# Optimization experiments

Hardware: AMD Instinct MI355X
Metric: run time of the kernel (lower is better)

The kernel has to match this reference:

```python
import jax, jax.numpy as jnp
import numpy as np

N_NODES = 100000
N_EDGES = 3200000
N_GRAPHS = 1000
HID = 64
L = 4  # num_unit


def setup_inputs() -> dict:
    key = jax.random.key(0)
    ks = jax.random.split(key, 16)
    x = jax.random.normal(ks[0], (N_NODES, 4), dtype=jnp.float32)
    edge_index = jax.random.randint(ks[1], (2, N_EDGES), 0, N_NODES, dtype=jnp.int64)
    edge_attr = jax.random.uniform(ks[2], (N_EDGES,), dtype=jnp.float32)
    batch = jnp.sort(jax.random.randint(ks[3], (N_NODES,), 0, N_GRAPHS, dtype=jnp.int64))
    s = 1.0 / np.sqrt(HID)
    inp = {
        'x': x, 'edge_index': edge_index, 'edge_attr': edge_attr, 'batch': batch,
        'emb_w': jax.random.normal(ks[4], (4, HID), jnp.float32) * 0.5,
        'emb_b': jnp.zeros((HID,), jnp.float32),
        'conv_w1': jax.random.normal(ks[5], (L, HID, HID), jnp.float32) * s,
        'conv_b1': jnp.zeros((L, HID), jnp.float32),
        'conv_w2': jax.random.normal(ks[6], (L, HID, HID), jnp.float32) * s,
        'conv_w3': jax.random.normal(ks[7], (L, HID, HID), jnp.float32) * s,
        'conv_b3': jnp.zeros((L, HID), jnp.float32),
        'lin1_w': jax.random.normal(ks[8], (HID, HID), jnp.float32) * s,
        'lin1_b': jnp.zeros((HID,), jnp.float32),
        'lin2_w': jax.random.normal(ks[9], (HID, 3), jnp.float32) * s,
        'lin2_b': jnp.zeros((3,), jnp.float32),
    }
    return inp


def _forward(x, edge_index, edge_attr, batch,
             emb_w, emb_b, conv_w1, conv_b1, conv_w2, conv_w3, conv_b3,
             lin1_w, lin1_b, lin2_w, lin2_b):
    src, dst = edge_index[0], edge_index[1]
    ew = edge_attr[:, None]  # [E,1]
    h = x @ emb_w + emb_b  # node_emb; dropout omitted (eval mode)
    for l in range(conv_w1.shape[0]):
        # LEConv: out_i = sum_{j->i} w_ji * (lin1(x_j) - lin2(x_i)) + lin3(x_i)
        a = h @ conv_w1[l] + conv_b1[l]
        b = h @ conv_w2[l]  # no bias
        msg = (a[src] - b[dst]) * ew  # [E, HID]
        agg = jax.ops.segment_sum(msg, dst, num_segments=h.shape[0])
        h = jax.nn.relu(agg + h @ conv_w3[l] + conv_b3[l])
    # global mean pool over graphs
    sums = jax.ops.segment_sum(h, batch, num_segments=N_GRAPHS)
    cnt = jax.ops.segment_sum(jnp.ones((h.shape[0],), h.dtype), batch, num_segments=N_GRAPHS)
    graph_x = sums / jnp.maximum(cnt, 1.0)[:, None]
    pred = jax.nn.relu(graph_x @ lin1_w + lin1_b) @ lin2_w + lin2_b
    return pred


def reference(x, edge_index, edge_attr, batch, emb_w, emb_b,
              conv_w1, conv_b1, conv_w2, conv_w3, conv_b3,
              lin1_w, lin1_b, lin2_w, lin2_b):
    return _forward(x, edge_index, edge_attr, batch, emb_w, emb_b,
                    conv_w1, conv_b1, conv_w2, conv_w3, conv_b3,
                    lin1_w, lin1_b, lin2_w, lin2_b)
```

## Files before the change

kernel.cpp:

```cpp
#include <hip/hip_runtime.h>

#define N_NODES 100000
#define N_EDGES 3200000
#define N_GRAPHS 1000
#define NLAYER 4
#define NB 391
#define G1 782
#define EPB 4096
#define PCAP 16384

typedef __attribute__((ext_vector_type(8))) short bf16x8;
typedef __attribute__((ext_vector_type(4))) float f32x4;

static __device__ __forceinline__ unsigned f2bf(float f) {
  unsigned u = __float_as_uint(f);
  return (u + 0x7fffu + ((u >> 16) & 1u)) >> 16;
}

__global__ __launch_bounds__(256) void embed_kernel(
    const float* __restrict__ x, const float* __restrict__ emb_w,
    const float* __restrict__ emb_b, float* __restrict__ h,
    unsigned short* __restrict__ h_bf)
{
  int t = blockIdx.x * 256 + threadIdx.x;
  if (t >= N_NODES * 64) return;
  int c = t & 63, v = t >> 6;
  float4 xv = ((const float4*)x)[v];
  float acc = emb_b[c];
  acc = fmaf(xv.x, emb_w[0 * 64 + c], acc);
  acc = fmaf(xv.y, emb_w[1 * 64 + c], acc);
  acc = fmaf(xv.z, emb_w[2 * 64 + c], acc);
  acc = fmaf(xv.w, emb_w[3 * 64 + c], acc);
  h[t] = acc;
  h_bf[t] = (unsigned short)f2bf(acc);
}

__global__ __launch_bounds__(256) void bhist_kernel(
    const int* __restrict__ ei, int* __restrict__ bhist)
{
  __shared__ unsigned hist[NB];
  for (int i = threadIdx.x; i < NB; i += 256) hist[i] = 0;
  __syncthreads();
  int base = blockIdx.x * EPB;
#pragma unroll
  for (int i = 0; i < 16; ++i) {
    int e = base + i * 256 + threadIdx.x;
    if (e < N_EDGES) atomicAdd(&hist[((unsigned)ei[N_EDGES + e]) >> 8], 1u);
  }
  __syncthreads();
  for (int i = threadIdx.x; i < NB; i += 256)
    bhist[blockIdx.x * NB + i] = (int)hist[i];
}

__global__ __launch_bounds__(256) void colscan_kernel(
    int* __restrict__ bhist, int* __restrict__ tots)
{
  int b = blockIdx.x;
  __shared__ int s[256];
  __shared__ int carry;
  if (threadIdx.x == 0) carry = 0;
  __syncthreads();
  for (int c0 = 0; c0 < G1; c0 += 256) {
    int g = c0 + threadIdx.x;
    int v = (g < G1) ? bhist[g * NB + b] : 0;
    s[threadIdx.x] = v;
    __syncthreads();
    for (int off = 1; off < 256; off <<= 1) {
      int y = (threadIdx.x >= off) ? s[threadIdx.x - off] : 0;
      __syncthreads();
      s[threadIdx.x] += y;
      __syncthreads();
    }
    if (g < G1) bhist[g * NB + b] = carry + s[threadIdx.x] - v;
    __syncthreads();
    if (threadIdx.x == 0) carry += s[255];
    __syncthreads();
  }
  if (threadIdx.x == 0) tots[b] = carry;
}

__global__ __launch_bounds__(512) void bucketscan_kernel(
    const int* __restrict__ tots, int* __restrict__ bb)
{
  __shared__ int s[512];
  int x = ((int)threadIdx.x < NB) ? tots[threadIdx.x] : 0;
  s[threadIdx.x] = x;
  __syncthreads();
  for (int off = 1; off < 512; off <<= 1) {
    int y = (threadIdx.x >= off) ? s[threadIdx.x - off] : 0;
    __syncthreads();
    s[threadIdx.x] += y;
    __syncthreads();
  }
  if ((int)threadIdx.x < NB) bb[threadIdx.x] = s[threadIdx.x] - x;
  if (threadIdx.x == 0) bb[NB] = N_EDGES;
}

__global__ __launch_bounds__(256) void bscatter_kernel(
    const int* __restrict__ ei, const float* __restrict__ ea,
    const int* __restrict__ bhist, const int* __restrict__ bb,
    int2* __restrict__ tmp)
{
  __shared__ unsigned hist[NB];
  __shared__ int lbase[NB];
  __shared__ unsigned cur[NB];
  __shared__ int2 stage[EPB];
  __shared__ unsigned short bid[EPB];
  __shared__ int carry;
  __shared__ int sbuf[256];
  int tid = threadIdx.x;
  int base = blockIdx.x * EPB;

  for (int i = tid; i < NB; i += 256) hist[i] = 0;
  if (tid == 0) carry = 0;
  __syncthreads();

#pragma unroll
  for (int i = 0; i < 16; ++i) {
    int e = base + i * 256 + tid;
    if (e < N_EDGES) atomicAdd(&hist[((unsigned)ei[N_EDGES + e]) >> 8], 1u);
  }
  __syncthreads();

  for (int c0 = 0; c0 < NB; c0 += 256) {
    int g = c0 + tid;
    int v = (g < NB) ? (int)hist[g] : 0;
    sbuf[tid] = v;
    __syncthreads();
    for (int off = 1; off < 256; off <<= 1) {
      int y = (tid >= off) ? sbuf[tid - off] : 0;
      __syncthreads();
      sbuf[tid] += y;
      __syncthreads();
    }
    if (g < NB) {
      int ex = carry + sbuf[tid] - v;
      lbase[g] = ex;
      cur[g] = (unsigned)ex;
    }
    __syncthreads();
    if (tid == 0) carry += sbuf[255];
    __syncthreads();
  }

#pragma unroll
  for (int i = 0; i < 16; ++i) {
    int e = base + i * 256 + tid;
    if (e < N_EDGES) {
      int d = ei[N_EDGES + e];
      unsigned bkt = ((unsigned)d) >> 8;
      unsigned lp = atomicAdd(&cur[bkt], 1u);
      stage[lp] = make_int2(ei[e] | ((d & 255) << 17), __float_as_int(ea[e]));
      bid[lp] = (unsigned short)bkt;
    }
  }
  __syncthreads();

  int nE = min(EPB, N_EDGES - base);
  for (int i = tid; i < nE; i += 256) {
    int bkt = (int)bid[i];
    int gpos = bb[bkt] + bhist[blockIdx.x * NB + bkt] + (i - lbase[bkt]);
    tmp[gpos] = stage[i];
  }
}

__global__ __launch_bounds__(256) void bucket_sort_kernel(
    const int* __restrict__ bb, const int2* __restrict__ tmp,
    int2* __restrict__ csr, int* __restrict__ row_off, float* __restrict__ degw)
{
  int j = blockIdx.x;
  int b0 = bb[j], b1 = bb[j + 1];
  int nE = b1 - b0;
  __shared__ unsigned hist[256];
  __shared__ float dws[256];
  __shared__ int scanbuf[256];
  __shared__ unsigned cur[256];
  __shared__ unsigned short perm[PCAP];
  int t = threadIdx.x;
  hist[t] = 0;
  dws[t] = 0.f;
  __syncthreads();
  for (int i = t; i < nE; i += 256) {
    int2 r = tmp[b0 + i];
    int bin = ((unsigned)r.x) >> 17;
    atomicAdd(&hist[bin], 1u);
    atomicAdd(&dws[bin], __int_as_float(r.y));
  }
  __syncthreads();
  int v = (int)hist[t];
  scanbuf[t] = v;
  __syncthreads();
  for (int off = 1; off < 256; off <<= 1) {
    int y = (t >= off) ? scanbuf[t - off] : 0;
    __syncthreads();
    scanbuf[t] += y;
    __syncthreads();
  }
  int myexcl = scanbuf[t] - v;
  cur[t] = (unsigned)myexcl;
  int vnode = (j << 8) + t;
  if (vnode < N_NODES) {
    row_off[vnode] = b0 + myexcl;
    degw[vnode] = dws[t];
  }
  if (j == NB - 1 && t == 0) row_off[N_NODES] = N_EDGES;
  __syncthreads();

  if (nE <= PCAP) {
    for (int i = t; i < nE; i += 256) {
      int2 r = tmp[b0 + i];
      int bin = ((unsigned)r.x) >> 17;
      unsigned p = atomicAdd(&cur[bin], 1u);
      perm[p] = (unsigned short)i;
    }
    __syncthreads();
    for (int q = t; q < nE; q += 256) {
      int2 r = tmp[b0 + (int)perm[q]];
      csr[b0 + q] = make_int2(r.x & 0x1FFFF, r.y);
    }
  } else {
    for (int i = t; i < nE; i += 256) {
      int2 r = tmp[b0 + i];
      int bin = ((unsigned)r.x) >> 17;
      unsigned p = atomicAdd(&cur[bin], 1u);
      csr[b0 + (int)p] = make_int2(r.x & 0x1FFFF, r.y);
    }
  }
}

__global__ __launch_bounds__(256) void matvec3_mfma_kernel(
    const unsigned short* __restrict__ h_bf,
    const float* __restrict__ w1, const float* __restrict__ b1,
    const float* __restrict__ w2,
    const float* __restrict__ w3, const float* __restrict__ b3,
    const float* __restrict__ degw,
    unsigned short* __restrict__ a_bf, float* __restrict__ cc_out)
{
  __shared__ unsigned wfrag[6144];
  int tid = threadIdx.x;
  {
    const float* wm0 = w2;
    const float* wm1 = w3;
    const float* wm2 = w1;
    for (int u = tid; u < 6144; u += 256) {
      int j2 = u & 3;
      int lane = (u >> 2) & 63;
      int t = (u >> 8) & 3;
      int c = (u >> 10) & 1;
      int m = u >> 11;
      int k = c * 32 + (lane >> 4) * 8 + j2 * 2;
      int n = t * 16 + (lane & 15);
      const float* W = (m == 0) ? wm0 : (m == 1) ? wm1 : wm2;
      unsigned lo = f2bf(W[k * 64 + n]);
      unsigned hi = f2bf(W[(k + 1) * 64 + n]);
      wfrag[u] = lo | (hi << 16);
    }
  }
  __syncthreads();

  int wave = tid >> 6;
  int lane = tid & 63;
  int quad = lane >> 4;
  int col = lane & 15;
  int nb = blockIdx.x * 64 + wave * 16;

  int arow = nb + col;
  if (arow >= N_NODES) arow = N_NODES - 1;
  const bf16x8* ap = (const bf16x8*)(h_bf + (size_t)arow * 64 + quad * 8);
  bf16x8 af0 = ap[0];
  bf16x8 af1 = ap[4];

  float dwr[4];
#pragma unroll
  for (int r = 0; r < 4; ++r) {
    int row = nb + quad * 4 + r;
    dwr[r] = degw[row < N_NODES ? row : 0];
  }

#pragma unroll
  for (int t = 0; t < 4; ++t) {
    const bf16x8* b20 = (const bf16x8*)&wfrag[((0 * 4 + t) << 8) + lane * 4];
    const bf16x8* b21 = (const bf16x8*)&wfrag[((1 * 4 + t) << 8) + lane * 4];
    const bf16x8* b30 = (const bf16x8*)&wfrag[((2 * 4 + t) << 8) + lane * 4];
    const bf16x8* b31 = (const bf16x8*)&wfrag[((3 * 4 + t) << 8) + lane * 4];
    const bf16x8* b10 = (const bf16x8*)&wfrag[((4 * 4 + t) << 8) + lane * 4];
    const bf16x8* b11 = (const bf16x8*)&wfrag[((5 * 4 + t) << 8) + lane * 4];

    f32x4 z = {0.f, 0.f, 0.f, 0.f};
    f32x4 acc2 = __builtin_amdgcn_mfma_f32_16x16x32_bf16(af0, *b20, z, 0, 0, 0);
    acc2 = __builtin_amdgcn_mfma_f32_16x16x32_bf16(af1, *b21, acc2, 0, 0, 0);
    f32x4 cc;
#pragma unroll
    for (int r = 0; r < 4; ++r) cc[r] = -dwr[r] * acc2[r];
    cc = __builtin_amdgcn_mfma_f32_16x16x32_bf16(af0, *b30, cc, 0, 0, 0);
    cc = __builtin_amdgcn_mfma_f32_16x16x32_bf16(af1, *b31, cc, 0, 0, 0);
    float bb3 = b3[t * 16 + col];
#pragma unroll
    for (int r = 0; r < 4; ++r) {
      int row = nb + quad * 4 + r;
      if (row < N_NODES) cc_out[(size_t)row * 64 + t * 16 + col] = cc[r] + bb3;
    }

    float bb1 = b1[t * 16 + col];
    f32x4 a1 = {bb1, bb1, bb1, bb1};
    a1 = __builtin_amdgcn_mfma_f32_16x16x32_bf16(af0, *b10, a1, 0, 0, 0);
    a1 = __builtin_amdgcn_mfma_f32_16x16x32_bf16(af1, *b11, a1, 0, 0, 0);
#pragma unroll
    for (int r = 0; r < 4; ++r) {
      int row = nb + quad * 4 + r;
      if (row < N_NODES)
        a_bf[(size_t)row * 64 + t * 16 + col] = (unsigned short)f2bf(a1[r]);
    }
  }
}

__global__ __launch_bounds__(256) void agg_kernel(
    const uint2* __restrict__ a2, const float4* __restrict__ cc4,
    const int* __restrict__ row_off, const int2* __restrict__ csr,
    float4* __restrict__ h4, unsigned short* __restrict__ h_bf)
{
  int wave = (blockIdx.x * 256 + threadIdx.x) >> 6;
  int lane = threadIdx.x & 63;
  int sg = lane >> 4;
  int li = lane & 15;
  int v = wave * 4 + sg;
  bool valid = v < N_NODES;
  int vc = valid ? v : N_NODES - 1;
  int base = row_off[vc];
  int ecnt = valid ? (row_off[vc + 1] - base) : 0;
  int emax = ecnt;
  emax = max(emax, __shfl_xor(emax, 16));
  emax = max(emax, __shfl_xor(emax, 32));

  float4 acc = valid ? cc4[(size_t)vc * 16 + li] : make_float4(0.f, 0.f, 0.f, 0.f);

  int full = emax & ~15;
  int c0 = 0;
  for (; c0 < full; c0 += 16) {
    int idx = c0 + li;
    int2 er = (idx < ecnt) ? csr[base + idx] : make_int2(0, 0);
#pragma unroll
    for (int j = 0; j < 16; ++j) {
      int sl = sg * 16 + j;
      int s = __shfl(er.x, sl);
      float w = __int_as_float(__shfl(er.y, sl));
      uint2 u = a2[(size_t)s * 16 + li];
      acc.x = fmaf(w, __uint_as_float(u.x << 16), acc.x);
      acc.y = fmaf(w, __uint_as_float(u.x & 0xffff0000u), acc.y);
      acc.z = fmaf(w, __uint_as_float(u.y << 16), acc.z);
      acc.w = fmaf(w, __uint_as_float(u.y & 0xffff0000u), acc.w);
    }
  }
  int rem = emax - full;
  if (rem > 0) {
    int idx = c0 + li;
    int2 er = (idx < ecnt) ? csr[base + idx] : make_int2(0, 0);
    for (int j = 0; j < rem; ++j) {
      int sl = sg * 16 + j;
      int s = __shfl(er.x, sl);
      float w = __int_as_float(__shfl(er.y, sl));
      uint2 u = a2[(size_t)s * 16 + li];
      acc.x = fmaf(w, __uint_as_float(u.x << 16), acc.x);
      acc.y = fmaf(w, __uint_as_float(u.x & 0xffff0000u), acc.y);
      acc.z = fmaf(w, __uint_as_float(u.y << 16), acc.z);
      acc.w = fmaf(w, __uint_as_float(u.y & 0xffff0000u), acc.w);
    }
  }
  if (valid) {
    acc.x = fmaxf(acc.x, 0.f);
    acc.y = fmaxf(acc.y, 0.f);
    acc.z = fmaxf(acc.z, 0.f);
    acc.w = fmaxf(acc.w, 0.f);
    h4[(size_t)v * 16 + li] = acc;
    uint2 p;
    p.x = f2bf(acc.x) | (f2bf(acc.y) << 16);
    p.y = f2bf(acc.z) | (f2bf(acc.w) << 16);
    ((uint2*)h_bf)[(size_t)v * 16 + li] = p;
  }
}

__global__ __launch_bounds__(256) void head_kernel(
    const float* __restrict__ h, const int* __restrict__ batch,
    const float* __restrict__ l1w, const float* __restrict__ l1b,
    const float* __restrict__ l2w, const float* __restrict__ l2b,
    float* __restrict__ out)
{
  int g = (blockIdx.x * 256 + threadIdx.x) >> 6;
  int lane = threadIdx.x & 63;
  if (g >= N_GRAPHS) return;
  int lo = 0, hi = N_NODES;
  while (lo < hi) { int mid = (lo + hi) >> 1; if (batch[mid] < g) lo = mid + 1; else hi = mid; }
  int start = lo;
  hi = N_NODES;
  while (lo < hi) { int mid = (lo + hi) >> 1; if (batch[mid] < g + 1) lo = mid + 1; else hi = mid; }
  int end = lo;

  float sum = 0.f;
  for (int v = start; v < end; ++v) sum += h[(size_t)v * 64 + lane];
  float cntf = (float)(end - start);
  float gx = sum / fmaxf(cntf, 1.f);

  float acc = l1b[lane];
  for (int k = 0; k < 64; ++k) {
    float gxk = __shfl(gx, k);
    acc = fmaf(gxk, l1w[k * 64 + lane], acc);
  }
  float t = fmaxf(acc, 0.f);
  float p0 = t * l2w[lane * 3 + 0];
  float p1 = t * l2w[lane * 3 + 1];
  float p2 = t * l2w[lane * 3 + 2];
  for (int off = 32; off > 0; off >>= 1) {
    p0 += __shfl_down(p0, off);
    p1 += __shfl_down(p1, off);
    p2 += __shfl_down(p2, off);
  }
  if (lane == 0) {
    out[g * 3 + 0] = p0 + l2b[0];
    out[g * 3 + 1] = p1 + l2b[1];
    out[g * 3 + 2] = p2 + l2b[2];
  }
}

extern "C" void kernel_launch(void* const* d_in, const int* in_sizes, int n_in,
                              void* d_out, int out_size, void* d_ws, size_t ws_size,
                              hipStream_t stream)
{
  (void)in_sizes; (void)n_in; (void)out_size; (void)ws_size;
  const float* x     = (const float*)d_in[0];
  const int*   ei    = (const int*)d_in[1];
  const float* ea    = (const float*)d_in[2];
  const int*   batch = (const int*)d_in[3];
  const float* emb_w = (const float*)d_in[4];
  const float* emb_b = (const float*)d_in[5];
  const float* cw1   = (const float*)d_in[6];
  const float* cb1   = (const float*)d_in[7];
  const float* cw2   = (const float*)d_in[8];
  const float* cw3   = (const float*)d_in[9];
  const float* cb3   = (const float*)d_in[10];
  const float* l1w   = (const float*)d_in[11];
  const float* l1b   = (const float*)d_in[12];
  const float* l2w   = (const float*)d_in[13];
  const float* l2b   = (const float*)d_in[14];
  float* out = (float*)d_out;

  char* wsb = (char*)d_ws;
  size_t off = 0;
  auto alloc = [&](size_t bytes) {
    char* p = wsb + off;
    off = (off + bytes + 255) & ~(size_t)255;
    return p;
  };
  float* h       = (float*)alloc(sizeof(float) * (size_t)N_NODES * 64);
  unsigned short* h_bf = (unsigned short*)alloc(sizeof(short) * (size_t)N_NODES * 64);
  unsigned short* a_bf = (unsigned short*)alloc(sizeof(short) * (size_t)N_NODES * 64);
  float* cc_buf  = (float*)alloc(sizeof(float) * (size_t)N_NODES * 64);
  int2*  csr     = (int2*)alloc(sizeof(int2) * (size_t)N_EDGES);
  int*   row_off = (int*)alloc(sizeof(int) * (N_NODES + 1));
  float* degw    = (float*)alloc(sizeof(float) * N_NODES);
  int*   bhist   = (int*)alloc(sizeof(int) * (size_t)G1 * NB);
  int*   tots    = (int*)alloc(sizeof(int) * NB);
  int*   bb      = (int*)alloc(sizeof(int) * (NB + 1));
  int2* tmp = (int2*)cc_buf;

  embed_kernel<<<(N_NODES * 64 + 255) / 256, 256, 0, stream>>>(x, emb_w, emb_b, h, h_bf);
  bhist_kernel<<<G1, 256, 0, stream>>>(ei, bhist);
  colscan_kernel<<<NB, 256, 0, stream>>>(bhist, tots);
  bucketscan_kernel<<<1, 512, 0, stream>>>(tots, bb);
  bscatter_kernel<<<G1, 256, 0, stream>>>(ei, ea, bhist, bb, tmp);
  bucket_sort_kernel<<<NB, 256, 0, stream>>>(bb, tmp, csr, row_off, degw);

  int agg_blocks = (N_NODES + 15) / 16;
  int mv_blocks = (N_NODES + 63) / 64;
  for (int l = 0; l < NLAYER; ++l) {
    matvec3_mfma_kernel<<<mv_blocks, 256, 0, stream>>>(
        h_bf, cw1 + l * 4096, cb1 + l * 64, cw2 + l * 4096, cw3 + l * 4096,
        cb3 + l * 64, degw, a_bf, cc_buf);
    agg_kernel<<<agg_blocks, 256, 0, stream>>>(
        (const uint2*)a_bf, (const float4*)cc_buf, row_off, csr, (float4*)h, h_bf);
  }

  head_kernel<<<(N_GRAPHS * 64 + 255) / 256, 256, 0, stream>>>(
      h, batch, l1w, l1b, l2w, l2b, out);
}
```

Before: 625.4 us.

## Pack CSR edges into 32-bit words, store cc in bf16, trim fp32 h writes

Each CSR edge is packed into one 32-bit word: a 17-bit source index plus the edge weight quantized to 15 bits. This halves the edge-stream bytes read per layer. The cc buffer is stored as bf16 instead of fp32, and the fp32 h is written only in the last layer. The matvec kernel now covers 256 rows per block to amortize the weight-fragment setup, and that setup loop is restructured for coalesced weight reads. The 15-bit weight quantization and bf16 cc add precision loss relative to the fp32 reference, which may affect tolerance.

```diff
diff --git a/kernel.cpp b/kernel.cpp
--- a/kernel.cpp
+++ b/kernel.cpp
@@ -16,11 +16,16 @@
   unsigned u = __float_as_uint(f);
   return (u + 0x7fffu + ((u >> 16) & 1u)) >> 16;
 }
+static __device__ __forceinline__ float bf2f_lo(unsigned u) {
+  return __uint_as_float(u << 16);
+}
+static __device__ __forceinline__ float bf2f_hi(unsigned u) {
+  return __uint_as_float(u & 0xffff0000u);
+}
 
 __global__ __launch_bounds__(256) void embed_kernel(
     const float* __restrict__ x, const float* __restrict__ emb_w,
-    const float* __restrict__ emb_b, float* __restrict__ h,
-    unsigned short* __restrict__ h_bf)
+    const float* __restrict__ emb_b, unsigned short* __restrict__ h_bf)
 {
   int t = blockIdx.x * 256 + threadIdx.x;
   if (t >= N_NODES * 64) return;
@@ -31,7 +36,6 @@
   acc = fmaf(xv.y, emb_w[1 * 64 + c], acc);
   acc = fmaf(xv.z, emb_w[2 * 64 + c], acc);
   acc = fmaf(xv.w, emb_w[3 * 64 + c], acc);
-  h[t] = acc;
   h_bf[t] = (unsigned short)f2bf(acc);
 }
 
@@ -166,7 +170,7 @@
 
 __global__ __launch_bounds__(256) void bucket_sort_kernel(
     const int* __restrict__ bb, const int2* __restrict__ tmp,
-    int2* __restrict__ csr, int* __restrict__ row_off, float* __restrict__ degw)
+    unsigned* __restrict__ csr, int* __restrict__ row_off, float* __restrict__ degw)
 {
   int j = blockIdx.x;
   int b0 = bb[j], b1 = bb[j + 1];
@@ -216,14 +220,16 @@
     __syncthreads();
     for (int q = t; q < nE; q += 256) {
       int2 r = tmp[b0 + (int)perm[q]];
-      csr[b0 + q] = make_int2(r.x & 0x1FFFF, r.y);
+      unsigned q15 = (unsigned)(__int_as_float(r.y) * 32768.0f);
+      csr[b0 + q] = ((unsigned)r.x & 0x1FFFFu) | (q15 << 17);
     }
   } else {
     for (int i = t; i < nE; i += 256) {
       int2 r = tmp[b0 + i];
       int bin = ((unsigned)r.x) >> 17;
       unsigned p = atomicAdd(&cur[bin], 1u);
-      csr[b0 + (int)p] = make_int2(r.x & 0x1FFFF, r.y);
+      unsigned q15 = (unsigned)(__int_as_float(r.y) * 32768.0f);
+      csr[b0 + (int)p] = ((unsigned)r.x & 0x1FFFFu) | (q15 << 17);
     }
   }
 }
@@ -234,26 +240,27 @@
     const float* __restrict__ w2,
     const float* __restrict__ w3, const float* __restrict__ b3,
     const float* __restrict__ degw,
-    unsigned short* __restrict__ a_bf, float* __restrict__ cc_out)
+    unsigned short* __restrict__ a_bf, unsigned short* __restrict__ cc_bf)
 {
   __shared__ unsigned wfrag[6144];
   int tid = threadIdx.x;
   {
-    const float* wm0 = w2;
-    const float* wm1 = w3;
-    const float* wm2 = w1;
-    for (int u = tid; u < 6144; u += 256) {
-      int j2 = u & 3;
-      int lane = (u >> 2) & 63;
-      int t = (u >> 8) & 3;
-      int c = (u >> 10) & 1;
-      int m = u >> 11;
-      int k = c * 32 + (lane >> 4) * 8 + j2 * 2;
-      int n = t * 16 + (lane & 15);
-      const float* W = (m == 0) ? wm0 : (m == 1) ? wm1 : wm2;
+    int n = tid & 63;
+    int gofs = tid >> 6;
+    for (int it = 0; it < 24; ++it) {
+      int g = it * 4 + gofs;
+      int m = g >> 5;
+      int kp = g & 31;
+      int k = kp * 2;
+      const float* W = (m == 0) ? w2 : (m == 1) ? w3 : w1;
       unsigned lo = f2bf(W[k * 64 + n]);
       unsigned hi = f2bf(W[(k + 1) * 64 + n]);
-      wfrag[u] = lo | (hi << 16);
+      int c = k >> 5;
+      int kk = k & 31;
+      int lane = ((kk >> 3) << 4) | (n & 15);
+      int j2 = (kk & 7) >> 1;
+      int t = n >> 4;
+      wfrag[(((m * 2 + c) * 4 + t) << 8) | (lane << 2) | j2] = lo | (hi << 16);
     }
   }
   __syncthreads();
@@ -262,62 +269,66 @@
   int lane = tid & 63;
   int quad = lane >> 4;
   int col = lane & 15;
-  int nb = blockIdx.x * 64 + wave * 16;
-
-  int arow = nb + col;
-  if (arow >= N_NODES) arow = N_NODES - 1;
-  const bf16x8* ap = (const bf16x8*)(h_bf + (size_t)arow * 64 + quad * 8);
-  bf16x8 af0 = ap[0];
-  bf16x8 af1 = ap[4];
-
-  float dwr[4];
-#pragma unroll
-  for (int r = 0; r < 4; ++r) {
-    int row = nb + quad * 4 + r;
-    dwr[r] = degw[row < N_NODES ? row : 0];
-  }
-
-#pragma unroll
-  for (int t = 0; t < 4; ++t) {
-    const bf16x8* b20 = (const bf16x8*)&wfrag[((0 * 4 + t) << 8) + lane * 4];
-    const bf16x8* b21 = (const bf16x8*)&wfrag[((1 * 4 + t) << 8) + lane * 4];
-    const bf16x8* b30 = (const bf16x8*)&wfrag[((2 * 4 + t) << 8) + lane * 4];
-    const bf16x8* b31 = (const bf16x8*)&wfrag[((3 * 4 + t) << 8) + lane * 4];
-    const bf16x8* b10 = (const bf16x8*)&wfrag[((4 * 4 + t) << 8) + lane * 4];
-    const bf16x8* b11 = (const bf16x8*)&wfrag[((5 * 4 + t) << 8) + lane * 4];
-
-    f32x4 z = {0.f, 0.f, 0.f, 0.f};
-    f32x4 acc2 = __builtin_amdgcn_mfma_f32_16x16x32_bf16(af0, *b20, z, 0, 0, 0);
-    acc2 = __builtin_amdgcn_mfma_f32_16x16x32_bf16(af1, *b21, acc2, 0, 0, 0);
-    f32x4 cc;
-#pragma unroll
-    for (int r = 0; r < 4; ++r) cc[r] = -dwr[r] * acc2[r];
-    cc = __builtin_amdgcn_mfma_f32_16x16x32_bf16(af0, *b30, cc, 0, 0, 0);
-    cc = __builtin_amdgcn_mfma_f32_16x16x32_bf16(af1, *b31, cc, 0, 0, 0);
-    float bb3 = b3[t * 16 + col];
+
+#pragma unroll
+  for (int tt = 0; tt < 4; ++tt) {
+    int nb = blockIdx.x * 256 + wave * 64 + tt * 16;
+    int arow = nb + col;
+    if (arow >= N_NODES) arow = N_NODES - 1;
+    const bf16x8* ap = (const bf16x8*)(h_bf + (size_t)arow * 64 + quad * 8);
+    bf16x8 af0 = ap[0];
+    bf16x8 af1 = ap[4];
+
+    float dwr[4];
 #pragma unroll
     for (int r = 0; r < 4; ++r) {
       int row = nb + quad * 4 + r;
-      if (row < N_NODES) cc_out[(size_t)row * 64 + t * 16 + col] = cc[r] + bb3;
-    }
-
-    float bb1 = b1[t * 16 + col];
-    f32x4 a1 = {bb1, bb1, bb1, bb1};
-    a1 = __builtin_amdgcn_mfma_f32_16x16x32_bf16(af0, *b10, a1, 0, 0, 0);
-    a1 = __builtin_amdgcn_mfma_f32_16x16x32_bf16(af1, *b11, a1, 0, 0, 0);
-#pragma unroll
-    for (int r = 0; r < 4; ++r) {
-      int row = nb + quad * 4 + r;
-      if (row < N_NODES)
-        a_bf[(size_t)row * 64 + t * 16 + col] = (unsigned short)f2bf(a1[r]);
+      dwr[r] = degw[row < N_NODES ? row : 0];
+    }
+
+#pragma unroll
+    for (int t = 0; t < 4; ++t) {
+      const bf16x8* b20 = (const bf16x8*)&wfrag[((0 * 4 + t) << 8) + lane * 4];
+      const bf16x8* b21 = (const bf16x8*)&wfrag[((1 * 4 + t) << 8) + lane * 4];
+      const bf16x8* b30 = (const bf16x8*)&wfrag[((2 * 4 + t) << 8) + lane * 4];
+      const bf16x8* b31 = (const bf16x8*)&wfrag[((3 * 4 + t) << 8) + lane * 4];
+      const bf16x8* b10 = (const bf16x8*)&wfrag[((4 * 4 + t) << 8) + lane * 4];
+      const bf16x8* b11 = (const bf16x8*)&wfrag[((5 * 4 + t) << 8) + lane * 4];
+
+      f32x4 z = {0.f, 0.f, 0.f, 0.f};
+      f32x4 acc2 = __builtin_amdgcn_mfma_f32_16x16x32_bf16(af0, *b20, z, 0, 0, 0);
+      acc2 = __builtin_amdgcn_mfma_f32_16x16x32_bf16(af1, *b21, acc2, 0, 0, 0);
+      f32x4 cc;
+#pragma unroll
+      for (int r = 0; r < 4; ++r) cc[r] = -dwr[r] * acc2[r];
+      cc = __builtin_amdgcn_mfma_f32_16x16x32_bf16(af0, *b30, cc, 0, 0, 0);
+      cc = __builtin_amdgcn_mfma_f32_16x16x32_bf16(af1, *b31, cc, 0, 0, 0);
+      float bb3 = b3[t * 16 + col];
+#pragma unroll
+      for (int r = 0; r < 4; ++r) {
+        int row = nb + quad * 4 + r;
+        if (row < N_NODES)
+          cc_bf[(size_t)row * 64 + t * 16 + col] = (unsigned short)f2bf(cc[r] + bb3);
+      }
+
+      float bb1 = b1[t * 16 + col];
+      f32x4 a1 = {bb1, bb1, bb1, bb1};
+      a1 = __builtin_amdgcn_mfma_f32_16x16x32_bf16(af0, *b10, a1, 0, 0, 0);
+      a1 = __builtin_amdgcn_mfma_f32_16x16x32_bf16(af1, *b11, a1, 0, 0, 0);
+#pragma unroll
+      for (int r = 0; r < 4; ++r) {
+        int row = nb + quad * 4 + r;
+        if (row < N_NODES)
+          a_bf[(size_t)row * 64 + t * 16 + col] = (unsigned short)f2bf(a1[r]);
+      }
     }
   }
 }
 
 __global__ __launch_bounds__(256) void agg_kernel(
-    const uint2* __restrict__ a2, const float4* __restrict__ cc4,
-    const int* __restrict__ row_off, const int2* __restrict__ csr,
-    float4* __restrict__ h4, unsigned short* __restrict__ h_bf)
+    const uint2* __restrict__ a2, const uint2* __restrict__ cc2,
+    const int* __restrict__ row_off, const unsigned* __restrict__ csr,
+    float4* __restrict__ h4, unsigned short* __restrict__ h_bf, int write_h)
 {
   int wave = (blockIdx.x * 256 + threadIdx.x) >> 6;
   int lane = threadIdx.x & 63;
@@ -332,38 +343,45 @@
   emax = max(emax, __shfl_xor(emax, 16));
   emax = max(emax, __shfl_xor(emax, 32));
 
-  float4 acc = valid ? cc4[(size_t)vc * 16 + li] : make_float4(0.f, 0.f, 0.f, 0.f);
+  float4 acc = make_float4(0.f, 0.f, 0.f, 0.f);
+  if (valid) {
+    uint2 cu = cc2[(size_t)vc * 16 + li];
+    acc.x = bf2f_lo(cu.x);
+    acc.y = bf2f_hi(cu.x);
+    acc.z = bf2f_lo(cu.y);
+    acc.w = bf2f_hi(cu.y);
+  }
 
   int full = emax & ~15;
   int c0 = 0;
   for (; c0 < full; c0 += 16) {
     int idx = c0 + li;
-    int2 er = (idx < ecnt) ? csr[base + idx] : make_int2(0, 0);
+    unsigned er = (idx < ecnt) ? csr[base + idx] : 0u;
 #pragma unroll
     for (int j = 0; j < 16; ++j) {
-      int sl = sg * 16 + j;
-      int s = __shfl(er.x, sl);
-      float w = __int_as_float(__shfl(er.y, sl));
+      unsigned r = (unsigned)__shfl((int)er, sg * 16 + j);
+      int s = (int)(r & 0x1FFFFu);
+      float w = (float)(r >> 17) * (1.0f / 32768.0f);
       uint2 u = a2[(size_t)s * 16 + li];
-      acc.x = fmaf(w, __uint_as_float(u.x << 16), acc.x);
-      acc.y = fmaf(w, __uint_as_float(u.x & 0xffff0000u), acc.y);
-      acc.z = fmaf(w, __uint_as_float(u.y << 16), acc.z);
-      acc.w = fmaf(w, __uint_as_float(u.y & 0xffff0000u), acc.w);
+      acc.x = fmaf(w, bf2f_lo(u.x), acc.x);
+      acc.y = fmaf(w, bf2f_hi(u.x), acc.y);
+      acc.z = fmaf(w, bf2f_lo(u.y), acc.z);
+      acc.w = fmaf(w, bf2f_hi(u.y), acc.w);
     }
   }
   int rem = emax - full;
   if (rem > 0) {
     int idx = c0 + li;
-    int2 er = (idx < ecnt) ? csr[base + idx] : make_int2(0, 0);
+    unsigned er = (idx < ecnt) ? csr[base + idx] : 0u;
     for (int j = 0; j < rem; ++j) {
-      int sl = sg * 16 + j;
-      int s = __shfl(er.x, sl);
-      float w = __int_as_float(__shfl(er.y, sl));
+      unsigned r = (unsigned)__shfl((int)er, sg * 16 + j);
+      int s = (int)(r & 0x1FFFFu);
+      float w = (float)(r >> 17) * (1.0f / 32768.0f);
       uint2 u = a2[(size_t)s * 16 + li];
-      acc.x = fmaf(w, __uint_as_float(u.x << 16), acc.x);
-      acc.y = fmaf(w, __uint_as_float(u.x & 0xffff0000u), acc.y);
-      acc.z = fmaf(w, __uint_as_float(u.y << 16), acc.z);
-      acc.w = fmaf(w, __uint_as_float(u.y & 0xffff0000u), acc.w);
+      acc.x = fmaf(w, bf2f_lo(u.x), acc.x);
+      acc.y = fmaf(w, bf2f_hi(u.x), acc.y);
+      acc.z = fmaf(w, bf2f_lo(u.y), acc.z);
+      acc.w = fmaf(w, bf2f_hi(u.y), acc.w);
     }
   }
   if (valid) {
@@ -371,7 +389,7 @@
     acc.y = fmaxf(acc.y, 0.f);
     acc.z = fmaxf(acc.z, 0.f);
     acc.w = fmaxf(acc.w, 0.f);
-    h4[(size_t)v * 16 + li] = acc;
+    if (write_h) h4[(size_t)v * 16 + li] = acc;
     uint2 p;
     p.x = f2bf(acc.x) | (f2bf(acc.y) << 16);
     p.y = f2bf(acc.z) | (f2bf(acc.w) << 16);
@@ -453,16 +471,16 @@
   float* h       = (float*)alloc(sizeof(float) * (size_t)N_NODES * 64);
   unsigned short* h_bf = (unsigned short*)alloc(sizeof(short) * (size_t)N_NODES * 64);
   unsigned short* a_bf = (unsigned short*)alloc(sizeof(short) * (size_t)N_NODES * 64);
-  float* cc_buf  = (float*)alloc(sizeof(float) * (size_t)N_NODES * 64);
-  int2*  csr     = (int2*)alloc(sizeof(int2) * (size_t)N_EDGES);
+  unsigned short* cc_bf = (unsigned short*)alloc(sizeof(short) * (size_t)N_NODES * 64);
+  unsigned* csr  = (unsigned*)alloc(sizeof(unsigned) * (size_t)N_EDGES);
   int*   row_off = (int*)alloc(sizeof(int) * (N_NODES + 1));
   float* degw    = (float*)alloc(sizeof(float) * N_NODES);
   int*   bhist   = (int*)alloc(sizeof(int) * (size_t)G1 * NB);
   int*   tots    = (int*)alloc(sizeof(int) * NB);
   int*   bb      = (int*)alloc(sizeof(int) * (NB + 1));
-  int2* tmp = (int2*)cc_buf;
-
-  embed_kernel<<<(N_NODES * 64 + 255) / 256, 256, 0, stream>>>(x, emb_w, emb_b, h, h_bf);
+  int2* tmp = (int2*)h;
+
+  embed_kernel<<<(N_NODES * 64 + 255) / 256, 256, 0, stream>>>(x, emb_w, emb_b, h_bf);
   bhist_kernel<<<G1, 256, 0, stream>>>(ei, bhist);
   colscan_kernel<<<NB, 256, 0, stream>>>(bhist, tots);
   bucketscan_kernel<<<1, 512, 0, stream>>>(tots, bb);
@@ -470,13 +488,14 @@
   bucket_sort_kernel<<<NB, 256, 0, stream>>>(bb, tmp, csr, row_off, degw);
 
   int agg_blocks = (N_NODES + 15) / 16;
-  int mv_blocks = (N_NODES + 63) / 64;
+  int mv_blocks = (N_NODES + 255) / 256;
   for (int l = 0; l < NLAYER; ++l) {
     matvec3_mfma_kernel<<<mv_blocks, 256, 0, stream>>>(
         h_bf, cw1 + l * 4096, cb1 + l * 64, cw2 + l * 4096, cw3 + l * 4096,
-        cb3 + l * 64, degw, a_bf, cc_buf);
+        cb3 + l * 64, degw, a_bf, cc_bf);
     agg_kernel<<<agg_blocks, 256, 0, stream>>>(
-        (const uint2*)a_bf, (const float4*)cc_buf, row_off, csr, (float4*)h, h_bf);
+        (const uint2*)a_bf, (const uint2*)cc_bf, row_off, csr, (float4*)h,
+        h_bf, (l == NLAYER - 1) ? 1 : 0);
   }
 
   head_kernel<<<(N_GRAPHS * 64 + 255) / 256, 256, 0, stream>>>(
```

After: 537.9 us. 1.16x faster.
